# Kernel tuning notes

Hardware: AMD Instinct MI355X
Metric: run time of the kernel (lower is better)

The kernel has to match this reference:

```python
import jax, jax.numpy as jnp
import numpy as np

H, DK, DIM, DFF, DEPTH = 8, 64, 512, 2048, 8
B, LS, LT, VOCAB = 16, 128, 128, 32000


def setup_inputs() -> dict:
    key = jax.random.key(0)
    ks = jax.random.split(key, 20)
    w = lambda k, s: jax.random.normal(k, s, jnp.float32) * 0.02
    N_enc, N_dec = B * LS, B * LT
    base_s = np.arange(B) * LS
    base_t = np.arange(B) * LT
    i = np.arange(LS)
    j = np.arange(LT)
    # encoder self-attn: full bipartite within each sentence
    ee_src = (base_s[:, None, None] + i[None, :, None] + 0 * i[None, None, :]).reshape(-1)
    ee_dst = (base_s[:, None, None] + 0 * i[None, :, None] + i[None, None, :]).reshape(-1)
    # decoder self-attn: causal (key pos <= query pos)
    ii, jj = np.meshgrid(j, j, indexing='ij')  # ii = dst(query) pos, jj = src(key) pos
    m = jj <= ii
    dd_src = (base_t[:, None] + jj[m][None, :]).reshape(-1)
    dd_dst = (base_t[:, None] + ii[m][None, :]).reshape(-1)
    # cross-attn: enc node -> dec node, full within sentence
    ed_src = (base_s[:, None, None] + i[None, :, None] + 0 * j[None, None, :]).reshape(-1)
    ed_dst = (base_t[:, None, None] + 0 * i[None, :, None] + j[None, None, :]).reshape(-1)
    return {
        'emb_src': w(ks[0], (VOCAB, DIM)), 'emb_tgt': w(ks[1], (VOCAB, DIM)),
        'pos_emb': w(ks[2], (LS, DIM)), 'time_emb': w(ks[3], (DEPTH, DIM)),
        'Wqkv_e': w(ks[4], (DIM, 3 * DIM)), 'Wo_e': w(ks[5], (DIM, DIM)),
        'W1_e': w(ks[6], (DIM, DFF)), 'W2_e': w(ks[7], (DFF, DIM)),
        'Wqkv_d': w(ks[8], (DIM, 3 * DIM)), 'Wo_d': w(ks[9], (DIM, DIM)),
        'W1_d': w(ks[10], (DIM, DFF)), 'W2_d': w(ks[11], (DFF, DIM)),
        'Wq_x': w(ks[12], (DIM, DIM)), 'Wkv_x': w(ks[13], (DIM, 2 * DIM)),
        'Wo_x': w(ks[14], (DIM, DIM)), 'Wgen': w(ks[15], (DIM, VOCAB)),
        'src_tokens': jax.random.randint(ks[16], (N_enc,), 0, VOCAB, jnp.int32),
        'tgt_tokens': jax.random.randint(ks[17], (N_dec,), 0, VOCAB, jnp.int32),
        'src_pos': jnp.tile(jnp.arange(LS, dtype=jnp.int32), B),
        'tgt_pos': jnp.tile(jnp.arange(LT, dtype=jnp.int32), B),
        'ee_src': jnp.asarray(ee_src, jnp.int32), 'ee_dst': jnp.asarray(ee_dst, jnp.int32),
        'dd_src': jnp.asarray(dd_src, jnp.int32), 'dd_dst': jnp.asarray(dd_dst, jnp.int32),
        'ed_src': jnp.asarray(ed_src, jnp.int32), 'ed_dst': jnp.asarray(ed_dst, jnp.int32),
    }


def _ln(x):
    m = x.mean(-1, keepdims=True)
    v = ((x - m) ** 2).mean(-1, keepdims=True)
    return (x - m) * jax.lax.rsqrt(v + 1e-5)


def _attn(q, k, v, src, dst, n_dst):
    # q: [Nq,H,DK] (dst side), k/v: [Nk,H,DK] (src side); edge lists [E]
    # src_dot_dst -> scaled_exp -> scatter-sum (src_mul_edge + sum, copy_edge + sum), then wv/z
    s = jnp.exp(jnp.einsum('ehd,ehd->eh', k[src], q[dst]) / np.float32(np.sqrt(DK)))  # [E,H]
    wv = jax.ops.segment_sum(s[:, :, None] * v[src], dst, num_segments=n_dst)  # [Nq,H,DK]
    z = jax.ops.segment_sum(s, dst, num_segments=n_dst)  # [Nq,H]
    return (wv / (z[:, :, None] + 1e-9)).reshape(n_dst, DIM)


def reference(emb_src, emb_tgt, pos_emb, time_emb, Wqkv_e, Wo_e, W1_e, W2_e,
              Wqkv_d, Wo_d, W1_d, W2_d, Wq_x, Wkv_x, Wo_x, Wgen,
              src_tokens, tgt_tokens, src_pos, tgt_pos,
              ee_src, ee_dst, dd_src, dd_dst, ed_src, ed_dst):
    Ne, Nd = src_tokens.shape[0], tgt_tokens.shape[0]
    x_e = emb_src[src_tokens] + pos_emb[src_pos]
    x_d = emb_tgt[tgt_tokens] + pos_emb[tgt_pos]
    # encoder: MAX_DEPTH shared-weight iterations with time+pos enc re-added each step
    for t in range(DEPTH):
        xp = x_e + pos_emb[src_pos] + time_emb[t]
        q, k, v = jnp.split(xp @ Wqkv_e, 3, axis=-1)
        o = _attn(q.reshape(Ne, H, DK), k.reshape(Ne, H, DK), v.reshape(Ne, H, DK), ee_src, ee_dst, Ne)
        x_e = _ln(x_e + o @ Wo_e)
        x_e = _ln(x_e + jax.nn.relu(x_e @ W1_e) @ W2_e)
    # decoder: self-attn (causal dd) then cross-attn (ed) each iteration
    for t in range(DEPTH):
        xp = x_d + pos_emb[tgt_pos] + time_emb[t]
        q, k, v = jnp.split(xp @ Wqkv_d, 3, axis=-1)
        o = _attn(q.reshape(Nd, H, DK), k.reshape(Nd, H, DK), v.reshape(Nd, H, DK), dd_src, dd_dst, Nd)
        x_d = _ln(x_d + o @ Wo_d)
        qx = ((x_d + pos_emb[tgt_pos] + time_emb[t]) @ Wq_x).reshape(Nd, H, DK)
        kx, vx = jnp.split(x_e @ Wkv_x, 2, axis=-1)
        o = _attn(qx, kx.reshape(Ne, H, DK), vx.reshape(Ne, H, DK), ed_src, ed_dst, Nd)
        x_d = _ln(x_d + o @ Wo_x)
        x_d = _ln(x_d + jax.nn.relu(x_d @ W1_d) @ W2_d)
    return jax.nn.log_softmax(x_d @ Wgen, axis=-1)  # generator over dec nodes
```

## Files before the change

### kernel.cpp

```cpp
#include <hip/hip_runtime.h>
#include <hip/hip_bf16.h>
#include <math.h>

#define H 8
#define DK 64
#define DIM 512
#define DFF 2048
#define DEPTH 8
#define VOCAB 32000
#define NTOK 2048

typedef float f32x4 __attribute__((ext_vector_type(4)));
typedef short bf16x8 __attribute__((ext_vector_type(8)));

static __device__ __forceinline__ unsigned short f2bf(float f) {
    unsigned u = __float_as_uint(f);
    return (unsigned short)((u + 0x7FFFu + ((u >> 16) & 1u)) >> 16);
}

#define GLL(src, dst) __builtin_amdgcn_global_load_lds( \
    (const __attribute__((address_space(1))) unsigned int*)(src), \
    (__attribute__((address_space(3))) unsigned int*)(dst), 16, 0, 0)

static __device__ __forceinline__ void load_ln_stats(
    const float* __restrict__ stats, int base, int rows,
    float* Lm, float* Li, int tid, int nthr)
{
    for (int r = tid; r < rows; r += nthr) {
        float m = 0.f, inv = 1.f;
        if (stats) {
            const float* s = stats + (size_t)(base + r) * 16;
            float sum = 0.f, sq = 0.f;
#pragma unroll
            for (int b = 0; b < 8; b++) { sum += s[b * 2]; sq += s[b * 2 + 1]; }
            m = sum * (1.f / 512.f);
            float v = sq * (1.f / 512.f) - m * m;
            inv = 1.f / sqrtf(v + 1e-5f);
        }
        Lm[r] = m; Li[r] = inv;
    }
}

__global__ void embed_kernel(const float* __restrict__ emb, const int* __restrict__ tok,
                             const float* __restrict__ pos, const int* __restrict__ pidx,
                             float* __restrict__ out, int n4) {
    int idx = blockIdx.x * blockDim.x + threadIdx.x;
    if (idx >= n4) return;
    int i = idx >> 7, d = idx & 127;
    float4 a = ((const float4*)emb)[(size_t)tok[i] * 128 + d];
    float4 b = ((const float4*)pos)[(size_t)pidx[i] * 128 + d];
    ((float4*)out)[idx] = make_float4(a.x + b.x, a.y + b.y, a.z + b.z, a.w + b.w);
}

struct WD { const float* src; unsigned short* dst; int K; int N; int t0; int pad; };
struct WTab { WD d[12]; };

__global__ __launch_bounds__(256) void wconv_all(WTab tab) {
    __shared__ float t[32][33];
    const int bid = blockIdx.x;
    int w = 0;
#pragma unroll
    for (int i = 1; i < 12; i++) if (bid >= tab.d[i].t0) w = i;
    const float* W = tab.d[w].src;
    unsigned short* Wt = tab.d[w].dst;
    const int K = tab.d[w].K, N = tab.d[w].N;
    const int lt = bid - tab.d[w].t0;
    const int txc = N >> 5;
    const int n0 = (lt % txc) << 5, k0 = (lt / txc) << 5;
    const int tid = threadIdx.x;
    const int tx = tid & 31, ty = tid >> 5;
#pragma unroll
    for (int i = 0; i < 32; i += 8)
        t[ty + i][tx] = W[(size_t)(k0 + ty + i) * N + n0 + tx];
    __syncthreads();
#pragma unroll
    for (int i = 0; i < 32; i += 8)
        Wt[(size_t)(n0 + ty + i) * K + k0 + tx] = f2bf(t[tx][ty + i]);
}

template<int EPI, int BN>
__global__ __launch_bounds__(256) void gemm_rb(
    const float* __restrict__ Tf,
    const float* __restrict__ stats,
    const unsigned short* __restrict__ Bt,
    unsigned short* __restrict__ Cb,
    int M, int N, int K)
{
    constexpr int JN = BN / 32;
    __shared__ __align__(16) unsigned short Asm[128 * 64];
    __shared__ __align__(16) unsigned short Bsm[BN * 64];
    __shared__ float Lm[128], Li[128];
    const int tid = threadIdx.x;
    const int lane = tid & 63, wid = tid >> 6;
    const int m0 = blockIdx.y * 128, n0 = blockIdx.x * BN;
    const int wm = (wid >> 1) * 64, wn = (wid & 1) * (BN / 2);

    load_ln_stats(stats, m0, 128, Lm, Li, tid, 256);
    __syncthreads();

    f32x4 acc[4][JN];
#pragma unroll
    for (int i = 0; i < 4; i++)
#pragma unroll
        for (int j = 0; j < JN; j++) acc[i][j] = (f32x4){0.f, 0.f, 0.f, 0.f};

    for (int k0 = 0; k0 < K; k0 += 64) {
        if (k0) __syncthreads();
#pragma unroll
        for (int it = 0; it < BN / 32; it++) {
            int q = it * 256 + tid;
            int row = q >> 3;
            int cs = (q & 7) ^ (row & 7);
            GLL(Bt + (size_t)(n0 + row) * K + k0 + cs * 8, &Bsm[q * 8]);
        }
#pragma unroll
        for (int it = 0; it < 4; it++) {
            int q = it * 256 + tid;
            int row = q >> 3;
            int cs = q & 7;
            const float* s = Tf + (size_t)(m0 + row) * K + k0 + cs * 8;
            float4 u0 = *(const float4*)s, u1 = *(const float4*)(s + 4);
            float m = Lm[row], iv = Li[row];
            unsigned short c8[8];
            c8[0] = f2bf((u0.x - m) * iv); c8[1] = f2bf((u0.y - m) * iv);
            c8[2] = f2bf((u0.z - m) * iv); c8[3] = f2bf((u0.w - m) * iv);
            c8[4] = f2bf((u1.x - m) * iv); c8[5] = f2bf((u1.y - m) * iv);
            c8[6] = f2bf((u1.z - m) * iv); c8[7] = f2bf((u1.w - m) * iv);
            *(bf16x8*)&Asm[row * 64 + ((cs ^ (row & 7)) * 8)] = *(bf16x8*)c8;
        }
        __syncthreads();
#pragma unroll
        for (int kk = 0; kk < 2; kk++) {
            bf16x8 af[4], bfr[JN];
#pragma unroll
            for (int i = 0; i < 4; i++) {
                int rowA = wm + i * 16 + (lane & 15);
                int ca = (kk * 4 + (lane >> 4)) ^ (rowA & 7);
                af[i] = *(const bf16x8*)&Asm[rowA * 64 + ca * 8];
            }
#pragma unroll
            for (int j = 0; j < JN; j++) {
                int rowB = wn + j * 16 + (lane & 15);
                int cb = (kk * 4 + (lane >> 4)) ^ (rowB & 7);
                bfr[j] = *(const bf16x8*)&Bsm[rowB * 64 + cb * 8];
            }
#pragma unroll
            for (int i = 0; i < 4; i++)
#pragma unroll
                for (int j = 0; j < JN; j++)
                    acc[i][j] = __builtin_amdgcn_mfma_f32_16x16x32_bf16(af[i], bfr[j], acc[i][j], 0, 0, 0);
        }
    }
#pragma unroll
    for (int i = 0; i < 4; i++)
#pragma unroll
        for (int j = 0; j < JN; j++)
#pragma unroll
            for (int r = 0; r < 4; r++) {
                int row = m0 + wm + i * 16 + (lane >> 4) * 4 + r;
                int col = n0 + wn + j * 16 + (lane & 15);
                size_t idx = (size_t)row * N + col;
                float v = acc[i][j][r];
                if (EPI == 1) Cb[idx] = f2bf(fmaxf(v, 0.f));
                if (EPI == 3) Cb[idx] = f2bf(v);
            }
}

__global__ __launch_bounds__(256) void gemm_bb(
    const unsigned short* __restrict__ A,
    const unsigned short* __restrict__ Bt,
    const float* __restrict__ Tin,
    const float* __restrict__ statsIn,
    float* __restrict__ Tout,
    float* __restrict__ statsOut,
    int M, int K)
{
    __shared__ __align__(16) unsigned short Asm[32 * 64];
    __shared__ __align__(16) unsigned short Bsm[64 * 64];
    __shared__ float Lm[32], Li[32];
    __shared__ float sredS[4][32], sredQ[4][32];
    const int tid = threadIdx.x;
    const int lane = tid & 63, wid = tid >> 6;
    const int nb = blockIdx.x;
    const int m0 = blockIdx.y * 32, n0 = nb * 64;
    const int wn = wid * 16;

    load_ln_stats(statsIn, m0, 32, Lm, Li, tid, 256);
    __syncthreads();

    f32x4 acc[2];
#pragma unroll
    for (int i = 0; i < 2; i++) acc[i] = (f32x4){0.f, 0.f, 0.f, 0.f};

    for (int k0 = 0; k0 < K; k0 += 64) {
        if (k0) __syncthreads();
        {
            int q = tid;
            int row = q >> 3;
            int cs = (q & 7) ^ (row & 7);
            GLL(A + (size_t)(m0 + row) * K + k0 + cs * 8, &Asm[q * 8]);
        }
#pragma unroll
        for (int it = 0; it < 2; it++) {
            int q = it * 256 + tid;
            int row = q >> 3;
            int cs = (q & 7) ^ (row & 7);
            GLL(Bt + (size_t)(n0 + row) * K + k0 + cs * 8, &Bsm[q * 8]);
        }
        __syncthreads();
#pragma unroll
        for (int kd = 0; kd < 2; kd++) {
            int rowB = wn + (lane & 15);
            int cb = (kd * 4 + (lane >> 4)) ^ (rowB & 7);
            bf16x8 bfr = *(const bf16x8*)&Bsm[rowB * 64 + cb * 8];
#pragma unroll
            for (int i = 0; i < 2; i++) {
                int rowA = i * 16 + (lane & 15);
                int ca = (kd * 4 + (lane >> 4)) ^ (rowA & 7);
                bf16x8 af = *(const bf16x8*)&Asm[rowA * 64 + ca * 8];
                acc[i] = __builtin_amdgcn_mfma_f32_16x16x32_bf16(af, bfr, acc[i], 0, 0, 0);
            }
        }
    }
#pragma unroll
    for (int i = 0; i < 2; i++) {
#pragma unroll
        for (int r = 0; r < 4; r++) {
            int rl = i * 16 + (lane >> 4) * 4 + r;
            int row = m0 + rl;
            int col = n0 + wn + (lane & 15);
            size_t idx = (size_t)row * DIM + col;
            float rv = (Tin[idx] - Lm[rl]) * Li[rl];
            float v = acc[i][r] + rv;
            Tout[idx] = v;
            float s = v, q = v * v;
            s += __shfl_xor(s, 1); s += __shfl_xor(s, 2);
            s += __shfl_xor(s, 4); s += __shfl_xor(s, 8);
            q += __shfl_xor(q, 1); q += __shfl_xor(q, 2);
            q += __shfl_xor(q, 4); q += __shfl_xor(q, 8);
            if ((lane & 15) == 0) { sredS[wid][rl] = s; sredQ[wid][rl] = q; }
        }
    }
    __syncthreads();
    if (tid < 32) {
        int row = tid;
        float s = sredS[0][row] + sredS[1][row] + sredS[2][row] + sredS[3][row];
        float q = sredQ[0][row] + sredQ[1][row] + sredQ[2][row] + sredQ[3][row];
        statsOut[(size_t)(m0 + row) * 16 + nb * 2] = s;
        statsOut[(size_t)(m0 + row) * 16 + nb * 2 + 1] = q;
    }
}

template<int CAUSAL>
static __device__ __forceinline__ void attn_phase2_split(
    const unsigned short* Qs, const unsigned short* Ks, const unsigned short* Vt,
    unsigned short* Psw, float* dumpf,
    int qh, int wid, int lane, int tok0, int h,
    unsigned short* __restrict__ O)
{
    const int qg = wid & 3, kh = wid >> 2;
    bf16x8 qa[2];
#pragma unroll
    for (int kd = 0; kd < 2; kd++) {
        int qr = qg * 16 + (lane & 15);
        int ch = (kd * 4 + (lane >> 4)) ^ (qr & 7);
        qa[kd] = *(const bf16x8*)&Qs[qr * 64 + ch * 8];
    }
    int jn, kcn;
    if (!CAUSAL)      { jn = 4; kcn = 2; }
    else if (kh > qh) { jn = 0; kcn = 0; }
    else if (kh < qh) { jn = 4; kcn = 2; }
    else              { kcn = (qg >> 1) + 1; jn = kcn * 2; }

    float zr[4] = {0.f, 0.f, 0.f, 0.f};
    f32x4 oacc[4];
#pragma unroll
    for (int dt = 0; dt < 4; dt++) oacc[dt] = (f32x4){0.f, 0.f, 0.f, 0.f};

    if (jn > 0) {
        f32x4 sacc[4];
#pragma unroll
        for (int j = 0; j < 4; j++) sacc[j] = (f32x4){0.f, 0.f, 0.f, 0.f};
#pragma unroll 2
        for (int kd = 0; kd < 2; kd++) {
            for (int jj = 0; jj < jn; jj++) {
                int kr = kh * 64 + jj * 16 + (lane & 15);
                int ch = (kd * 4 + (lane >> 4)) ^ (kr & 7);
                bf16x8 kf = *(const bf16x8*)&Ks[kr * 64 + ch * 8];
                sacc[jj] = __builtin_amdgcn_mfma_f32_16x16x32_bf16(qa[kd], kf, sacc[jj], 0, 0, 0);
            }
        }
        int qbase = qh * 64 + qg * 16 + (lane >> 4) * 4;
        for (int jj = 0; jj < jn; jj++) {
            int kcol = kh * 64 + jj * 16 + (lane & 15);
#pragma unroll
            for (int rr = 0; rr < 4; rr++) {
                float p = __expf(sacc[jj][rr] * 0.125f);
                if (CAUSAL && kcol > qbase + rr) p = 0.f;
                zr[rr] += p;
                int prow = (lane >> 4) * 4 + rr;
                int ch = ((jj * 2 + ((lane & 15) >> 3)) ^ (prow & 7));
                Psw[prow * 64 + ch * 8 + (lane & 7)] = f2bf(p);
            }
        }
        for (int kcl = 0; kcl < kcn; kcl++) {
            bf16x8 pa;
            {
                int prow = lane & 15;
                int ch = (kcl * 4 + (lane >> 4)) ^ (prow & 7);
                pa = *(const bf16x8*)&Psw[prow * 64 + ch * 8];
            }
            int kcg = kh * 2 + kcl;
#pragma unroll
            for (int dt = 0; dt < 4; dt++) {
                int d = dt * 16 + (lane & 15);
                bf16x8 vf = *(const bf16x8*)&Vt[d * 132 + (kcg * 4 + (lane >> 4)) * 8];
                oacc[dt] = __builtin_amdgcn_mfma_f32_16x16x32_bf16(pa, vf, oacc[dt], 0, 0, 0);
            }
        }
    }
    __syncthreads();
    if (kh == 1) {
        float* dst = dumpf + (size_t)(qg * 64 + lane) * 20;
#pragma unroll
        for (int dt = 0; dt < 4; dt++)
#pragma unroll
            for (int rr = 0; rr < 4; rr++) dst[dt * 4 + rr] = oacc[dt][rr];
#pragma unroll
        for (int rr = 0; rr < 4; rr++) dst[16 + rr] = zr[rr];
    }
    __syncthreads();
    if (kh == 0) {
        const float* src = dumpf + (size_t)(qg * 64 + lane) * 20;
#pragma unroll
        for (int dt = 0; dt < 4; dt++)
#pragma unroll
            for (int rr = 0; rr < 4; rr++) oacc[dt][rr] += src[dt * 4 + rr];
#pragma unroll
        for (int rr = 0; rr < 4; rr++) {
            float z = zr[rr] + src[16 + rr];
            z += __shfl_xor(z, 1); z += __shfl_xor(z, 2);
            z += __shfl_xor(z, 4); z += __shfl_xor(z, 8);
            zr[rr] = 1.f / (z + 1e-9f);
        }
#pragma unroll
        for (int dt = 0; dt < 4; dt++)
#pragma unroll
            for (int rr = 0; rr < 4; rr++) {
                int qrow = tok0 + qh * 64 + qg * 16 + (lane >> 4) * 4 + rr;
                O[(size_t)qrow * DIM + h * 64 + dt * 16 + (lane & 15)] =
                    f2bf(oacc[dt][rr] * zr[rr]);
            }
    }
}

template<int CAUSAL>
__global__ __launch_bounds__(512) void fused_attn(
    const float* __restrict__ Tf,
    const float* __restrict__ stats,
    const float* __restrict__ pos,
    const float* __restrict__ trow,
    const unsigned short* __restrict__ WqkvT,
    unsigned short* __restrict__ O)
{
    __shared__ __align__(16) unsigned short smem[28928];
    __shared__ float LmA[128], LiA[128];
    unsigned short* Asm = smem;
    unsigned short* Bsm = smem + 8192;
    unsigned short* Qs  = smem;
    unsigned short* Ks  = smem + 4096;
    unsigned short* Vt  = smem + 12288;
    float* dumpf = (float*)smem;
    const int tid = threadIdx.x;
    const int lane = tid & 63, wid = tid >> 6;
    unsigned short* Psw = smem + 20736 + wid * 1024;
    const int blk = blockIdx.x;
    const int qh = blk & 1, h = (blk >> 1) & 7, b = blk >> 4;
    const int tok0 = b * 128;
    const int wr = wid * 16;

    load_ln_stats(stats, tok0, 128, LmA, LiA, tid, 512);
    __syncthreads();

    f32x4 acc[12];
#pragma unroll
    for (int c = 0; c < 12; c++) acc[c] = (f32x4){0.f, 0.f, 0.f, 0.f};

    for (int k0 = 0; k0 < 512; k0 += 64) {
        if (k0) __syncthreads();
#pragma unroll
        for (int it = 0; it < 3; it++) {
            int q = it * 512 + wid * 64 + lane;
            int r = q >> 3;
            int cs = (q & 7) ^ (r & 7);
            int srow = (r < 64) ? (h * 64 + r)
                     : (r < 128) ? (512 + h * 64 + (r - 64))
                                 : (1024 + h * 64 + (r - 128));
            GLL(WqkvT + (size_t)srow * 512 + k0 + cs * 8, &Bsm[(it * 512 + wid * 64) * 8]);
        }
#pragma unroll
        for (int it = 0; it < 2; it++) {
            int q = it * 512 + tid;
            int row = q >> 3;
            int cs = q & 7;
            const float* s = Tf + (size_t)(tok0 + row) * 512 + k0 + cs * 8;
            const float* pp = pos + (size_t)row * 512 + k0 + cs * 8;
            const float* tt = trow + k0 + cs * 8;
            float4 u0 = *(const float4*)s, u1 = *(const float4*)(s + 4);
            float4 p0 = *(const float4*)pp, p1 = *(const float4*)(pp + 4);
            float4 t0 = *(const float4*)tt, t1 = *(const float4*)(tt + 4);
            float m = LmA[row], iv = LiA[row];
            unsigned short c8[8];
            c8[0] = f2bf((u0.x - m) * iv + p0.x + t0.x);
            c8[1] = f2bf((u0.y - m) * iv + p0.y + t0.y);
            c8[2] = f2bf((u0.z - m) * iv + p0.z + t0.z);
            c8[3] = f2bf((u0.w - m) * iv + p0.w + t0.w);
            c8[4] = f2bf((u1.x - m) * iv + p1.x + t1.x);
            c8[5] = f2bf((u1.y - m) * iv + p1.y + t1.y);
            c8[6] = f2bf((u1.z - m) * iv + p1.z + t1.z);
            c8[7] = f2bf((u1.w - m) * iv + p1.w + t1.w);
            *(bf16x8*)&Asm[row * 64 + ((cs ^ (row & 7)) * 8)] = *(bf16x8*)c8;
        }
        __syncthreads();
#pragma unroll
        for (int kk = 0; kk < 2; kk++) {
            int rowA = wr + (lane & 15);
            int ca = (kk * 4 + (lane >> 4)) ^ (rowA & 7);
            bf16x8 af = *(const bf16x8*)&Asm[rowA * 64 + ca * 8];
#pragma unroll
            for (int c = 0; c < 12; c++) {
                int rowB = c * 16 + (lane & 15);
                int cb = (kk * 4 + (lane >> 4)) ^ (rowB & 7);
                bf16x8 bfr = *(const bf16x8*)&Bsm[rowB * 64 + cb * 8];
                acc[c] = __builtin_amdgcn_mfma_f32_16x16x32_bf16(af, bfr, acc[c], 0, 0, 0);
            }
        }
    }
    __syncthreads();
#pragma unroll
    for (int c = 0; c < 12; c++)
#pragma unroll
        for (int r = 0; r < 4; r++) {
            int token = wr + (lane >> 4) * 4 + r;
            int col = (c & 3) * 16 + (lane & 15);
            unsigned short v = f2bf(acc[c][r]);
            if (c < 4) {
                int tl = token - qh * 64;
                if (tl >= 0 && tl < 64)
                    Qs[tl * 64 + (((col >> 3) ^ (tl & 7)) * 8) + (col & 7)] = v;
            } else if (c < 8) {
                Ks[token * 64 + (((col >> 3) ^ (token & 7)) * 8) + (col & 7)] = v;
            } else {
                Vt[col * 132 + token] = v;
            }
        }
    __syncthreads();
    attn_phase2_split<CAUSAL>(Qs, Ks, Vt, Psw, dumpf, qh, wid, lane, tok0, h, O);
}

__global__ __launch_bounds__(512) void fused_xattn(
    const float* __restrict__ Tf,
    const float* __restrict__ stats,
    const float* __restrict__ pos,
    const float* __restrict__ trow,
    const unsigned short* __restrict__ WqT,
    const unsigned short* __restrict__ kvx,
    unsigned short* __restrict__ O)
{
    __shared__ __align__(16) unsigned short smem[28928];
    __shared__ float LmA[64], LiA[64];
    unsigned short* Qs  = smem;
    unsigned short* Ks  = smem + 4096;
    unsigned short* Vt  = smem + 12288;
    unsigned short* Asm = smem + 20736;
    unsigned short* Bsm = smem + 24832;
    float* dumpf = (float*)smem;
    const int tid = threadIdx.x;
    const int lane = tid & 63, wid = tid >> 6;
    unsigned short* Psw = smem + 20736 + wid * 1024;
    const int blk = blockIdx.x;
    const int qh = blk & 1, h = (blk >> 1) & 7, b = blk >> 4;
    const int tok0 = b * 128;

    load_ln_stats(stats, tok0 + qh * 64, 64, LmA, LiA, tid, 512);

    if (wid >= 4) {
        int st = tid - 256;
        int r = st >> 1, c0 = (st & 1) * 4;
        const unsigned short* Kg = kvx + (size_t)(tok0 + r) * 1024 + h * 64;
        const unsigned short* Vg = Kg + 512;
#pragma unroll
        for (int c = c0; c < c0 + 4; c++) {
            bf16x8 kv = *(const bf16x8*)&Kg[c * 8];
            *(bf16x8*)&Ks[r * 64 + ((c ^ (r & 7)) * 8)] = kv;
            bf16x8 vv = *(const bf16x8*)&Vg[c * 8];
#pragma unroll
            for (int j = 0; j < 8; j++)
                Vt[(c * 8 + j) * 132 + r] = (unsigned short)vv[j];
        }
    }
    __syncthreads();

    f32x4 acc[4];
#pragma unroll
    for (int c = 0; c < 4; c++) acc[c] = (f32x4){0.f, 0.f, 0.f, 0.f};

    for (int k0 = 0; k0 < 512; k0 += 64) {
        if (k0) __syncthreads();
        if (tid < 256) {
#pragma unroll
            for (int it = 0; it < 2; it++) {
                int q = it * 256 + tid;
                int r = q >> 3;
                int cs = (q & 7) ^ (r & 7);
                GLL(WqT + (size_t)(h * 64 + r) * 512 + k0 + cs * 8, &Bsm[q * 8]);
            }
#pragma unroll
            for (int it = 0; it < 2; it++) {
                int q = it * 256 + tid;
                int row = q >> 3;
                int cs = q & 7;
                const float* s = Tf + (size_t)(tok0 + qh * 64 + row) * 512 + k0 + cs * 8;
                const float* pp = pos + (size_t)(qh * 64 + row) * 512 + k0 + cs * 8;
                const float* tt = trow + k0 + cs * 8;
                float4 u0 = *(const float4*)s, u1 = *(const float4*)(s + 4);
                float4 p0 = *(const float4*)pp, p1 = *(const float4*)(pp + 4);
                float4 t0 = *(const float4*)tt, t1 = *(const float4*)(tt + 4);
                float m = LmA[row], iv = LiA[row];
                unsigned short c8[8];
                c8[0] = f2bf((u0.x - m) * iv + p0.x + t0.x);
                c8[1] = f2bf((u0.y - m) * iv + p0.y + t0.y);
                c8[2] = f2bf((u0.z - m) * iv + p0.z + t0.z);
                c8[3] = f2bf((u0.w - m) * iv + p0.w + t0.w);
                c8[4] = f2bf((u1.x - m) * iv + p1.x + t1.x);
                c8[5] = f2bf((u1.y - m) * iv + p1.y + t1.y);
                c8[6] = f2bf((u1.z - m) * iv + p1.z + t1.z);
                c8[7] = f2bf((u1.w - m) * iv + p1.w + t1.w);
                *(bf16x8*)&Asm[row * 64 + ((cs ^ (row & 7)) * 8)] = *(bf16x8*)c8;
            }
        }
        __syncthreads();
        if (wid < 4) {
#pragma unroll
            for (int kk = 0; kk < 2; kk++) {
                int rowA = wid * 16 + (lane & 15);
                int ca = (kk * 4 + (lane >> 4)) ^ (rowA & 7);
                bf16x8 af = *(const bf16x8*)&Asm[rowA * 64 + ca * 8];
#pragma unroll
                for (int c = 0; c < 4; c++) {
                    int rowB = c * 16 + (lane & 15);
                    int cb = (kk * 4 + (lane >> 4)) ^ (rowB & 7);
                    bf16x8 bfr = *(const bf16x8*)&Bsm[rowB * 64 + cb * 8];
                    acc[c] = __builtin_amdgcn_mfma_f32_16x16x32_bf16(af, bfr, acc[c], 0, 0, 0);
                }
            }
        }
    }
    __syncthreads();
    if (wid < 4) {
#pragma unroll
        for (int c = 0; c < 4; c++)
#pragma unroll
            for (int r = 0; r < 4; r++) {
                int tl = wid * 16 + (lane >> 4) * 4 + r;
                int col = c * 16 + (lane & 15);
                Qs[tl * 64 + (((col >> 3) ^ (tl & 7)) * 8) + (col & 7)] = f2bf(acc[c][r]);
            }
    }
    __syncthreads();
    attn_phase2_split<0>(Qs, Ks, Vt, Psw, dumpf, qh, wid, lane, tok0, h, O);
}

__global__ __launch_bounds__(64) void ln_fin(const float* __restrict__ T,
                                             const float* __restrict__ stats,
                                             unsigned short* __restrict__ outb) {
    const int row = blockIdx.x, lane = threadIdx.x;
    const float* st = stats + (size_t)row * 16;
    float sum = 0.f, sq = 0.f;
#pragma unroll
    for (int b = 0; b < 8; b++) { sum += st[b * 2]; sq += st[b * 2 + 1]; }
    float m = sum * (1.f / 512.f);
    float v = sq * (1.f / 512.f) - m * m;
    float inv = 1.f / sqrtf(v + 1e-5f);
    const float* p = T + (size_t)row * DIM;
    unsigned short* qb = outb + (size_t)row * DIM;
#pragma unroll
    for (int i = 0; i < 8; i++)
        qb[lane + i * 64] = f2bf((p[lane + i * 64] - m) * inv);
}

template<int PASS>
__global__ __launch_bounds__(512) void gemm_gen(
    const unsigned short* __restrict__ Ab,
    const unsigned short* __restrict__ Bt,
    float* __restrict__ Out,
    float* __restrict__ pm,
    float* __restrict__ psum,
    const float* __restrict__ lse)
{
    __shared__ __align__(16) unsigned short Asm[256 * 64];
    __shared__ __align__(16) unsigned short Bsm[128 * 64];
    __shared__ float pml[8][64];
    __shared__ float psl[8][64];
    __shared__ float lsh[256];
    const int tid = threadIdx.x;
    const int lane = tid & 63, wid = tid >> 6;
    const int d = blockIdx.x + blockIdx.y * 8;
    const int t = (d & 7) * 250 + (d >> 3);
    const int mt = t & 7, nt = t >> 3;
    const int m0 = mt * 256, n0 = nt * 128;
    const int wm = (wid >> 1) * 64, wn = (wid & 1) * 64;

    if (PASS == 1) {
        for (int r = tid; r < 256; r += 512) lsh[r] = lse[m0 + r];
        __syncthreads();
    }

    f32x4 acc[4][4];
#pragma unroll
    for (int i = 0; i < 4; i++)
#pragma unroll
        for (int j = 0; j < 4; j++) acc[i][j] = (f32x4){0.f, 0.f, 0.f, 0.f};

    for (int k0 = 0; k0 < 512; k0 += 64) {
        if (k0 || PASS == 1) __syncthreads();
#pragma unroll
        for (int it = 0; it < 2; it++) {
            int q = it * 512 + tid;
            int row = q >> 3;
            int cs = (q & 7) ^ (row & 7);
            GLL(Bt + (size_t)(n0 + row) * 512 + k0 + cs * 8, &Bsm[(it * 512 + wid * 64) * 8]);
        }
#pragma unroll
        for (int it = 0; it < 4; it++) {
            int q = it * 512 + tid;
            int row = q >> 3;
            int cs = (q & 7) ^ (row & 7);
            GLL(Ab + (size_t)(m0 + row) * 512 + k0 + cs * 8, &Asm[(it * 512 + wid * 64) * 8]);
        }
        __syncthreads();
#pragma unroll
        for (int kk = 0; kk < 2; kk++) {
            bf16x8 af[4], bfr[4];
#pragma unroll
            for (int i = 0; i < 4; i++) {
                int rowA = wm + i * 16 + (lane & 15);
                int ca = (kk * 4 + (lane >> 4)) ^ (rowA & 7);
                af[i] = *(const bf16x8*)&Asm[rowA * 64 + ca * 8];
                int rowB = wn + i * 16 + (lane & 15);
                int cb = (kk * 4 + (lane >> 4)) ^ (rowB & 7);
                bfr[i] = *(const bf16x8*)&Bsm[rowB * 64 + cb * 8];
            }
#pragma unroll
            for (int i = 0; i < 4; i++)
#pragma unroll
                for (int j = 0; j < 4; j++)
                    acc[i][j] = __builtin_amdgcn_mfma_f32_16x16x32_bf16(af[i], bfr[j], acc[i][j], 0, 0, 0);
        }
    }
    if (PASS == 0) {
#pragma unroll
        for (int i = 0; i < 4; i++) {
#pragma unroll
            for (int r = 0; r < 4; r++) {
                float mx = fmaxf(fmaxf(acc[i][0][r], acc[i][1][r]),
                                 fmaxf(acc[i][2][r], acc[i][3][r]));
                mx = fmaxf(mx, __shfl_xor(mx, 1));
                mx = fmaxf(mx, __shfl_xor(mx, 2));
                mx = fmaxf(mx, __shfl_xor(mx, 4));
                mx = fmaxf(mx, __shfl_xor(mx, 8));
                float s = __expf(acc[i][0][r] - mx) + __expf(acc[i][1][r] - mx) +
                          __expf(acc[i][2][r] - mx) + __expf(acc[i][3][r] - mx);
                s += __shfl_xor(s, 1); s += __shfl_xor(s, 2);
                s += __shfl_xor(s, 4); s += __shfl_xor(s, 8);
                if ((lane & 15) == 0) {
                    int li = i * 16 + (lane >> 4) * 4 + r;
                    pml[wid][li] = mx;
                    psl[wid][li] = s;
                }
            }
        }
        __syncthreads();
        if (tid < 256) {
            int g = tid >> 6, lr = tid & 63;
            int wa = g * 2, wb = g * 2 + 1;
            float m = fmaxf(pml[wa][lr], pml[wb][lr]);
            float s = psl[wa][lr] * __expf(pml[wa][lr] - m) + psl[wb][lr] * __expf(pml[wb][lr] - m);
            pm[(size_t)(m0 + g * 64 + lr) * 256 + nt] = m;
            psum[(size_t)(m0 + g * 64 + lr) * 256 + nt] = s;
        }
    } else {
#pragma unroll
        for (int i = 0; i < 4; i++)
#pragma unroll
            for (int j = 0; j < 4; j++)
#pragma unroll
                for (int r = 0; r < 4; r++) {
                    int rl = wm + i * 16 + (lane >> 4) * 4 + r;
                    int col = n0 + wn + j * 16 + (lane & 15);
                    Out[(size_t)(m0 + rl) * VOCAB + col] = acc[i][j][r] - lsh[rl];
                }
    }
}

__global__ __launch_bounds__(64) void lse_kernel(const float* __restrict__ pm,
                                                 const float* __restrict__ psum,
                                                 float* __restrict__ lse) {
    const int row = blockIdx.x, t = threadIdx.x;
    float m = -1e30f, s = 0.f;
    for (int nb = t; nb < 250; nb += 64) {
        float mm = pm[(size_t)row * 256 + nb];
        float ss = psum[(size_t)row * 256 + nb];
        float M = fmaxf(m, mm);
        s = s * __expf(m - M) + ss * __expf(mm - M);
        m = M;
    }
#pragma unroll
    for (int off = 32; off > 0; off >>= 1) {
        float mo = __shfl_xor(m, off), so = __shfl_xor(s, off);
        float M = fmaxf(m, mo);
        s = s * __expf(m - M) + so * __expf(mo - M);
        m = M;
    }
    if (t == 0) lse[row] = m + __logf(s);
}

extern "C" void kernel_launch(void* const* d_in, const int* in_sizes, int n_in,
                              void* d_out, int out_size, void* d_ws, size_t ws_size,
                              hipStream_t stream) {
    const float* emb_src  = (const float*)d_in[0];
    const float* emb_tgt  = (const float*)d_in[1];
    const float* pos_emb  = (const float*)d_in[2];
    const float* time_emb = (const float*)d_in[3];
    const float* Wqkv_e   = (const float*)d_in[4];
    const float* Wo_e     = (const float*)d_in[5];
    const float* W1_e     = (const float*)d_in[6];
    const float* W2_e     = (const float*)d_in[7];
    const float* Wqkv_d   = (const float*)d_in[8];
    const float* Wo_d     = (const float*)d_in[9];
    const float* W1_d     = (const float*)d_in[10];
    const float* W2_d     = (const float*)d_in[11];
    const float* Wq_x     = (const float*)d_in[12];
    const float* Wkv_x    = (const float*)d_in[13];
    const float* Wo_x     = (const float*)d_in[14];
    const float* Wgen     = (const float*)d_in[15];
    const int* src_tokens = (const int*)d_in[16];
    const int* tgt_tokens = (const int*)d_in[17];
    const int* src_pos    = (const int*)d_in[18];
    const int* tgt_pos    = (const int*)d_in[19];

    char* w = (char*)d_ws;
    float* T_e0 = (float*)(w);
    float* T_e1 = (float*)(w + (4u << 20));
    float* T_d0 = (float*)(w + (8u << 20));
    float* T_d1 = (float*)(w + (12u << 20));
    float* T_d2 = (float*)(w + (16u << 20));
    unsigned short* kvx_bf = (unsigned short*)(w + (20u << 20));
    unsigned short* o_bf   = (unsigned short*)(w + (24u << 20));
    unsigned short* hid_bf = (unsigned short*)(w + (26u << 20));
    unsigned short* xd_bf  = (unsigned short*)(w + (34u << 20));
    float* pm   = (float*)(w + (36u << 20));
    float* psum = (float*)(w + (38u << 20));
    float* se0  = (float*)(w + (40u << 20));
    float* se1  = se0 + 32768;
    float* sd0  = se1 + 32768;
    float* sd1  = sd0 + 32768;
    float* sd2  = sd1 + 32768;
    float* lse  = sd2 + 32768;
    unsigned short* wts = (unsigned short*)(w + (41u << 20));

    unsigned short* WqkvE_t = wts;
    unsigned short* WoE_t   = WqkvE_t + 786432;
    unsigned short* W1E_t   = WoE_t   + 262144;
    unsigned short* W2E_t   = W1E_t   + 1048576;
    unsigned short* WqkvD_t = W2E_t   + 1048576;
    unsigned short* WoD_t   = WqkvD_t + 786432;
    unsigned short* W1D_t   = WoD_t   + 262144;
    unsigned short* W2D_t   = W1D_t   + 1048576;
    unsigned short* WqX_t   = W2D_t   + 1048576;
    unsigned short* WkvX_t  = WqX_t   + 262144;
    unsigned short* WoX_t   = WkvX_t  + 524288;
    unsigned short* Wgen_t  = WoX_t   + 262144;

    float* out = (float*)d_out;

    WTab tab;
    auto set = [&](int i, const float* s, unsigned short* d, int K, int N, int t0) {
        tab.d[i].src = s; tab.d[i].dst = d; tab.d[i].K = K; tab.d[i].N = N;
        tab.d[i].t0 = t0; tab.d[i].pad = 0;
    };
    set(0,  Wqkv_e, WqkvE_t, 512, 1536, 0);
    set(1,  Wo_e,   WoE_t,   512, 512,  768);
    set(2,  W1_e,   W1E_t,   512, 2048, 1024);
    set(3,  W2_e,   W2E_t,   2048, 512, 2048);
    set(4,  Wqkv_d, WqkvD_t, 512, 1536, 3072);
    set(5,  Wo_d,   WoD_t,   512, 512,  3840);
    set(6,  W1_d,   W1D_t,   512, 2048, 4096);
    set(7,  W2_d,   W2D_t,   2048, 512, 5120);
    set(8,  Wq_x,   WqX_t,   512, 512,  6144);
    set(9,  Wkv_x,  WkvX_t,  512, 1024, 6400);
    set(10, Wo_x,   WoX_t,   512, 512,  6912);
    set(11, Wgen,   Wgen_t,  512, 32000, 7168);
    wconv_all<<<23168, 256, 0, stream>>>(tab);

    const int n4 = NTOK * (DIM / 4);
    dim3 eb(256), eg((n4 + 255) / 256);
    embed_kernel<<<eg, eb, 0, stream>>>(emb_src, src_tokens, pos_emb, src_pos, T_e0, n4);
    embed_kernel<<<eg, eb, 0, stream>>>(emb_tgt, tgt_tokens, pos_emb, tgt_pos, T_d0, n4);

    const dim3 gFF(DFF / 64, NTOK / 128),
               gKV(1024 / 64, NTOK / 128),
               gBB(8, NTOK / 32);

    {
        const float* scur = nullptr;
        for (int t = 0; t < DEPTH; t++) {
            const float* trow = time_emb + (size_t)t * DIM;
            fused_attn<0><<<256, 512, 0, stream>>>(T_e0, scur, pos_emb, trow, WqkvE_t, o_bf);
            gemm_bb<<<gBB, 256, 0, stream>>>(o_bf, WoE_t, T_e0, scur, T_e1, se0, NTOK, 512);
            gemm_rb<1, 64><<<gFF, 256, 0, stream>>>(T_e1, se0, W1E_t, hid_bf, NTOK, DFF, 512);
            gemm_bb<<<gBB, 256, 0, stream>>>(hid_bf, W2E_t, T_e1, se0, T_e0, se1, NTOK, 2048);
            scur = se1;
        }
    }

    gemm_rb<3, 64><<<gKV, 256, 0, stream>>>(T_e0, se1, WkvX_t, kvx_bf, NTOK, 1024, 512);

    {
        const float* scur = nullptr;
        for (int t = 0; t < DEPTH; t++) {
            const float* trow = time_emb + (size_t)t * DIM;
            fused_attn<1><<<256, 512, 0, stream>>>(T_d0, scur, pos_emb, trow, WqkvD_t, o_bf);
            gemm_bb<<<gBB, 256, 0, stream>>>(o_bf, WoD_t, T_d0, scur, T_d1, sd0, NTOK, 512);

            fused_xattn<<<256, 512, 0, stream>>>(T_d1, sd0, pos_emb, trow, WqX_t, kvx_bf, o_bf);
            gemm_bb<<<gBB, 256, 0, stream>>>(o_bf, WoX_t, T_d1, sd0, T_d2, sd1, NTOK, 512);

            gemm_rb<1, 64><<<gFF, 256, 0, stream>>>(T_d2, sd1, W1D_t, hid_bf, NTOK, DFF, 512);
            gemm_bb<<<gBB, 256, 0, stream>>>(hid_bf, W2D_t, T_d2, sd1, T_d0, sd2, NTOK, 2048);
            scur = sd2;
        }
    }

    ln_fin<<<NTOK, 64, 0, stream>>>(T_d0, sd2, xd_bf);
    gemm_gen<0><<<dim3(8, 250), 512, 0, stream>>>(xd_bf, Wgen_t, nullptr, pm, psum, nullptr);
    lse_kernel<<<NTOK, 64, 0, stream>>>(pm, psum, lse);
    gemm_gen<1><<<dim3(8, 250), 512, 0, stream>>>(xd_bf, Wgen_t, out, nullptr, nullptr, lse);
}
```

Baseline: 1.744 ms.

## Double-buffer LDS tiles in gemm_rb and gemm_bb to overlap loads with MFMA

Both GEMM kernels get ping-pong LDS buffers, so the next K-tile's global_load_lds (and, in gemm_rb, the fp32 A register prefetch) is issued before the current tile's MFMAs run. The LN-normalize and bf16 convert of A moves after the compute, and the loop needs only one barrier per iteration. This is meant to hide global memory latency behind matrix math. The cost is twice the LDS footprint and more registers held for the A prefetch, which may lower occupancy.

```diff
diff --git a/kernel.cpp b/kernel.cpp
--- a/kernel.cpp
+++ b/kernel.cpp
@@ -78,7 +78,7 @@
         Wt[(size_t)(n0 + ty + i) * K + k0 + tx] = f2bf(t[tx][ty + i]);
 }
 
-template<int EPI, int BN>
+template<int EPI>
 __global__ __launch_bounds__(256) void gemm_rb(
     const float* __restrict__ Tf,
     const float* __restrict__ stats,
@@ -86,49 +86,72 @@
     unsigned short* __restrict__ Cb,
     int M, int N, int K)
 {
-    constexpr int JN = BN / 32;
-    __shared__ __align__(16) unsigned short Asm[128 * 64];
-    __shared__ __align__(16) unsigned short Bsm[BN * 64];
+    constexpr int BN = 64, JN = 2;
+    __shared__ __align__(16) unsigned short Asm[2][128 * 64];
+    __shared__ __align__(16) unsigned short Bsm[2][BN * 64];
     __shared__ float Lm[128], Li[128];
     const int tid = threadIdx.x;
     const int lane = tid & 63, wid = tid >> 6;
     const int m0 = blockIdx.y * 128, n0 = blockIdx.x * BN;
     const int wm = (wid >> 1) * 64, wn = (wid & 1) * (BN / 2);
-
-    load_ln_stats(stats, m0, 128, Lm, Li, tid, 256);
-    __syncthreads();
-
-    f32x4 acc[4][JN];
-#pragma unroll
-    for (int i = 0; i < 4; i++)
-#pragma unroll
-        for (int j = 0; j < JN; j++) acc[i][j] = (f32x4){0.f, 0.f, 0.f, 0.f};
-
-    for (int k0 = 0; k0 < K; k0 += 64) {
-        if (k0) __syncthreads();
-#pragma unroll
-        for (int it = 0; it < BN / 32; it++) {
-            int q = it * 256 + tid;
-            int row = q >> 3;
-            int cs = (q & 7) ^ (row & 7);
-            GLL(Bt + (size_t)(n0 + row) * K + k0 + cs * 8, &Bsm[q * 8]);
-        }
+    const int NK = K >> 6;
+
+    float4 ar0[4], ar1[4];
+    auto loadA = [&](int k0) {
 #pragma unroll
         for (int it = 0; it < 4; it++) {
             int q = it * 256 + tid;
             int row = q >> 3;
             int cs = q & 7;
             const float* s = Tf + (size_t)(m0 + row) * K + k0 + cs * 8;
-            float4 u0 = *(const float4*)s, u1 = *(const float4*)(s + 4);
+            ar0[it] = *(const float4*)s;
+            ar1[it] = *(const float4*)(s + 4);
+        }
+    };
+    auto storeA = [&](int buf) {
+#pragma unroll
+        for (int it = 0; it < 4; it++) {
+            int q = it * 256 + tid;
+            int row = q >> 3;
+            int cs = q & 7;
             float m = Lm[row], iv = Li[row];
             unsigned short c8[8];
-            c8[0] = f2bf((u0.x - m) * iv); c8[1] = f2bf((u0.y - m) * iv);
-            c8[2] = f2bf((u0.z - m) * iv); c8[3] = f2bf((u0.w - m) * iv);
-            c8[4] = f2bf((u1.x - m) * iv); c8[5] = f2bf((u1.y - m) * iv);
-            c8[6] = f2bf((u1.z - m) * iv); c8[7] = f2bf((u1.w - m) * iv);
-            *(bf16x8*)&Asm[row * 64 + ((cs ^ (row & 7)) * 8)] = *(bf16x8*)c8;
-        }
+            c8[0] = f2bf((ar0[it].x - m) * iv); c8[1] = f2bf((ar0[it].y - m) * iv);
+            c8[2] = f2bf((ar0[it].z - m) * iv); c8[3] = f2bf((ar0[it].w - m) * iv);
+            c8[4] = f2bf((ar1[it].x - m) * iv); c8[5] = f2bf((ar1[it].y - m) * iv);
+            c8[6] = f2bf((ar1[it].z - m) * iv); c8[7] = f2bf((ar1[it].w - m) * iv);
+            *(bf16x8*)&Asm[buf][row * 64 + ((cs ^ (row & 7)) * 8)] = *(bf16x8*)c8;
+        }
+    };
+    auto stageB = [&](int k0, int buf) {
+#pragma unroll
+        for (int it = 0; it < BN / 32; it++) {
+            int q = it * 256 + tid;
+            int row = q >> 3;
+            int cs = (q & 7) ^ (row & 7);
+            GLL(Bt + (size_t)(n0 + row) * K + k0 + cs * 8, &Bsm[buf][q * 8]);
+        }
+    };
+
+    load_ln_stats(stats, m0, 128, Lm, Li, tid, 256);
+    loadA(0);
+    __syncthreads();
+    storeA(0);
+    stageB(0, 0);
+
+    f32x4 acc[4][JN];
+#pragma unroll
+    for (int i = 0; i < 4; i++)
+#pragma unroll
+        for (int j = 0; j < JN; j++) acc[i][j] = (f32x4){0.f, 0.f, 0.f, 0.f};
+
+    for (int kt = 0; kt < NK; kt++) {
         __syncthreads();
+        const int cur = kt & 1, nxt = (kt + 1) & 1;
+        if (kt + 1 < NK) {
+            stageB((kt + 1) << 6, nxt);
+            loadA((kt + 1) << 6);
+        }
 #pragma unroll
         for (int kk = 0; kk < 2; kk++) {
             bf16x8 af[4], bfr[JN];
@@ -136,13 +159,13 @@
             for (int i = 0; i < 4; i++) {
                 int rowA = wm + i * 16 + (lane & 15);
                 int ca = (kk * 4 + (lane >> 4)) ^ (rowA & 7);
-                af[i] = *(const bf16x8*)&Asm[rowA * 64 + ca * 8];
+                af[i] = *(const bf16x8*)&Asm[cur][rowA * 64 + ca * 8];
             }
 #pragma unroll
             for (int j = 0; j < JN; j++) {
                 int rowB = wn + j * 16 + (lane & 15);
                 int cb = (kk * 4 + (lane >> 4)) ^ (rowB & 7);
-                bfr[j] = *(const bf16x8*)&Bsm[rowB * 64 + cb * 8];
+                bfr[j] = *(const bf16x8*)&Bsm[cur][rowB * 64 + cb * 8];
             }
 #pragma unroll
             for (int i = 0; i < 4; i++)
@@ -150,6 +173,7 @@
                 for (int j = 0; j < JN; j++)
                     acc[i][j] = __builtin_amdgcn_mfma_f32_16x16x32_bf16(af[i], bfr[j], acc[i][j], 0, 0, 0);
         }
+        if (kt + 1 < NK) storeA(nxt);
     }
 #pragma unroll
     for (int i = 0; i < 4; i++)
@@ -175,8 +199,8 @@
     float* __restrict__ statsOut,
     int M, int K)
 {
-    __shared__ __align__(16) unsigned short Asm[32 * 64];
-    __shared__ __align__(16) unsigned short Bsm[64 * 64];
+    __shared__ __align__(16) unsigned short Asm[2][32 * 64];
+    __shared__ __align__(16) unsigned short Bsm[2][64 * 64];
     __shared__ float Lm[32], Li[32];
     __shared__ float sredS[4][32], sredQ[4][32];
     const int tid = threadIdx.x;
@@ -184,40 +208,45 @@
     const int nb = blockIdx.x;
     const int m0 = blockIdx.y * 32, n0 = nb * 64;
     const int wn = wid * 16;
-
-    load_ln_stats(statsIn, m0, 32, Lm, Li, tid, 256);
-    __syncthreads();
-
-    f32x4 acc[2];
-#pragma unroll
-    for (int i = 0; i < 2; i++) acc[i] = (f32x4){0.f, 0.f, 0.f, 0.f};
-
-    for (int k0 = 0; k0 < K; k0 += 64) {
-        if (k0) __syncthreads();
+    const int NK = K >> 6;
+
+    auto stage = [&](int k0, int buf) {
         {
             int q = tid;
             int row = q >> 3;
             int cs = (q & 7) ^ (row & 7);
-            GLL(A + (size_t)(m0 + row) * K + k0 + cs * 8, &Asm[q * 8]);
+            GLL(A + (size_t)(m0 + row) * K + k0 + cs * 8, &Asm[buf][q * 8]);
         }
 #pragma unroll
         for (int it = 0; it < 2; it++) {
             int q = it * 256 + tid;
             int row = q >> 3;
             int cs = (q & 7) ^ (row & 7);
-            GLL(Bt + (size_t)(n0 + row) * K + k0 + cs * 8, &Bsm[q * 8]);
-        }
+            GLL(Bt + (size_t)(n0 + row) * K + k0 + cs * 8, &Bsm[buf][q * 8]);
+        }
+    };
+
+    load_ln_stats(statsIn, m0, 32, Lm, Li, tid, 256);
+    stage(0, 0);
+
+    f32x4 acc[2];
+#pragma unroll
+    for (int i = 0; i < 2; i++) acc[i] = (f32x4){0.f, 0.f, 0.f, 0.f};
+
+    for (int kt = 0; kt < NK; kt++) {
         __syncthreads();
+        const int cur = kt & 1, nxt = (kt + 1) & 1;
+        if (kt + 1 < NK) stage((kt + 1) << 6, nxt);
 #pragma unroll
         for (int kd = 0; kd < 2; kd++) {
             int rowB = wn + (lane & 15);
             int cb = (kd * 4 + (lane >> 4)) ^ (rowB & 7);
-            bf16x8 bfr = *(const bf16x8*)&Bsm[rowB * 64 + cb * 8];
+            bf16x8 bfr = *(const bf16x8*)&Bsm[cur][rowB * 64 + cb * 8];
 #pragma unroll
             for (int i = 0; i < 2; i++) {
                 int rowA = i * 16 + (lane & 15);
                 int ca = (kd * 4 + (lane >> 4)) ^ (rowA & 7);
-                bf16x8 af = *(const bf16x8*)&Asm[rowA * 64 + ca * 8];
+                bf16x8 af = *(const bf16x8*)&Asm[cur][rowA * 64 + ca * 8];
                 acc[i] = __builtin_amdgcn_mfma_f32_16x16x32_bf16(af, bfr, acc[i], 0, 0, 0);
             }
         }
@@ -818,13 +847,13 @@
             const float* trow = time_emb + (size_t)t * DIM;
             fused_attn<0><<<256, 512, 0, stream>>>(T_e0, scur, pos_emb, trow, WqkvE_t, o_bf);
             gemm_bb<<<gBB, 256, 0, stream>>>(o_bf, WoE_t, T_e0, scur, T_e1, se0, NTOK, 512);
-            gemm_rb<1, 64><<<gFF, 256, 0, stream>>>(T_e1, se0, W1E_t, hid_bf, NTOK, DFF, 512);
+            gemm_rb<1><<<gFF, 256, 0, stream>>>(T_e1, se0, W1E_t, hid_bf, NTOK, DFF, 512);
             gemm_bb<<<gBB, 256, 0, stream>>>(hid_bf, W2E_t, T_e1, se0, T_e0, se1, NTOK, 2048);
             scur = se1;
         }
     }
 
-    gemm_rb<3, 64><<<gKV, 256, 0, stream>>>(T_e0, se1, WkvX_t, kvx_bf, NTOK, 1024, 512);
+    gemm_rb<3><<<gKV, 256, 0, stream>>>(T_e0, se1, WkvX_t, kvx_bf, NTOK, 1024, 512);
 
     {
         const float* scur = nullptr;
@@ -836,7 +865,7 @@
             fused_xattn<<<256, 512, 0, stream>>>(T_d1, sd0, pos_emb, trow, WqX_t, kvx_bf, o_bf);
             gemm_bb<<<gBB, 256, 0, stream>>>(o_bf, WoX_t, T_d1, sd0, T_d2, sd1, NTOK, 512);
 
-            gemm_rb<1, 64><<<gFF, 256, 0, stream>>>(T_d2, sd1, W1D_t, hid_bf, NTOK, DFF, 512);
+            gemm_rb<1><<<gFF, 256, 0, stream>>>(T_d2, sd1, W1D_t, hid_bf, NTOK, DFF, 512);
             gemm_bb<<<gBB, 256, 0, stream>>>(hid_bf, W2D_t, T_d2, sd1, T_d0, sd2, NTOK, 2048);
             scur = sd2;
         }
```

After: 1.688 ms. 1.03x faster.
